# Kernel optimization log

Measured on AMD Instinct MI355X. Metric: run time of the kernel, lower is better.

The kernel has to match this reference:

```python
import jax, jax.numpy as jnp
import numpy as np

B, L, N, M = 2, 4, 2048, 1024
K, DIV = 32, 4
S = K // DIV  # maxpool window along neighbor axis
F1 = 128      # prev features
PF = 64       # lift output point-feature dim
OUT = 256
EPS = 1e-5


def setup_inputs() -> dict:
    key = jax.random.key(0)
    ks = jax.random.split(key, 12)
    C_in = PF + F1  # 192, conv input channels
    return {
        "points": jax.random.normal(ks[0], (B, L, N, 3), jnp.float32),
        "queries": jax.random.normal(ks[1], (B, L, M, 3), jnp.float32),
        "feat_prev": jax.random.normal(ks[2], (B, L, N, F1), jnp.float32),
        # Lift params
        "bn1_g": jnp.ones((3,), jnp.float32),
        "bn1_b": jnp.zeros((3,), jnp.float32),
        "w1": jax.random.normal(ks[3], (PF // 2, 3), jnp.float32) * 0.3,
        "b1": jnp.zeros((PF // 2,), jnp.float32),
        "bn2_g": jnp.ones((PF // 2,), jnp.float32),
        "bn2_b": jnp.zeros((PF // 2,), jnp.float32),
        "w2": jax.random.normal(ks[4], (PF, PF // 2), jnp.float32) * 0.1,
        "b2": jnp.zeros((PF,), jnp.float32),
        # conv = BatchNorm3d(C_in) + Conv3d(C_in, OUT, (1,1,DIV))
        "bnc_g": jnp.ones((C_in,), jnp.float32),
        "bnc_b": jnp.zeros((C_in,), jnp.float32),
        "conv_w": jax.random.normal(ks[5], (OUT, C_in, DIV), jnp.float32) * 0.05,
        "conv_b": jnp.zeros((OUT,), jnp.float32),
    }


def _bn(x, g, b):
    """Training-mode batchnorm, channel = last axis (equivalent to the
    torch transpose(1,4)->BatchNorm3d->transpose(1,4) pattern)."""
    ax = tuple(range(x.ndim - 1))
    m = x.mean(ax)
    v = x.var(ax)  # biased variance, as torch uses for normalization
    return (x - m) * jax.lax.rsqrt(v + EPS) * g + b


_gather = jax.vmap(jax.vmap(lambda arr, idx: arr[idx]))  # over B, L


def reference(points, queries, feat_prev,
              bn1_g, bn1_b, w1, b1, bn2_g, bn2_b, w2, b2,
              bnc_g, bnc_b, conv_w, conv_b):
    # ---- KNN (cdist + topk, fully batched) ----
    pn = jnp.sum(points * points, -1)          # (B,L,N)
    qn = jnp.sum(queries * queries, -1)        # (B,L,M)
    cross = jnp.einsum('blmc,blnc->blmn', queries, points)
    d2 = qn[..., None] + pn[:, :, None, :] - 2.0 * cross  # (B,L,M,N)
    idx = jax.lax.top_k(-d2, K)[1]             # (B,L,M,K) ascending distance

    nn_pts = _gather(points, idx)              # (B,L,M,K,3)
    local = queries[:, :, :, None, :] - nn_pts # center - neighbors

    # ---- Lift MLP (with batchnorm) ----
    h = _bn(local, bn1_g, bn1_b)
    h = jax.nn.relu(jnp.einsum('blmki,oi->blmko', h, w1) + b1)
    h = _bn(h, bn2_g, bn2_b)
    h = jax.nn.relu(jnp.einsum('blmki,oi->blmko', h, w2) + b2)  # (B,L,M,K,PF)

    # ---- gather prev features, concat ----
    fp = _gather(feat_prev, idx)               # (B,L,M,K,F1)
    feat = jnp.concatenate([h, fp], axis=-1)   # (B,L,M,K,C_in)

    # ---- maxpool over neighbor shells: window S, stride S along K ----
    C = feat.shape[-1]
    fm = feat.reshape(B, L, M, DIV, S, C).max(axis=4)  # (B,L,M,DIV,C)

    # ---- BatchNorm3d(C_in) + Conv3d(C_in, OUT, (1,1,DIV)) ----
    fm = _bn(fm, bnc_g, bnc_b)
    out = jnp.einsum('blmdc,ocd->blmo', fm, conv_w) + conv_b  # (B,L,M,OUT)
    return out
```

## Files before the change

kernel.cpp:

```cpp
#include <hip/hip_runtime.h>
#include <cstdint>

#define B_    2
#define L_    4
#define N_    2048
#define M_    1024
#define K_    32
#define DIV_  4
#define S_    8
#define F1_   128
#define PF_   64
#define CIN_  192
#define OUT_  256
#define EPS_  1e-5f

#define BL_   (B_*L_)
#define BLM_  (BL_*M_)
#define NPTS_ (BLM_*K_)
#define ROWS_ (BLM_*DIV_)

#define OFF_FMH  0
#define OFF_IDX  3145728
#define OFF_LOC  3407872
#define OFF_W1F  4456448
#define OFF_B1F  4456544
#define OFF_W2F  4456576
#define OFF_B2F  4458624
#define OFF_WCB  4458688
#define OFF_BCF  4556992
#define OFF_P2   4557248
#define OFF_P3   4573632

typedef __attribute__((ext_vector_type(8))) short short8;
typedef __attribute__((ext_vector_type(4))) short short4v;
typedef __attribute__((ext_vector_type(4))) float f32x4;

__device__ __forceinline__ unsigned short f2bf(float f)
{
    unsigned u = __float_as_uint(f);
    unsigned r = (u + 0x7FFFu + ((u >> 16) & 1u)) >> 16;
    return (unsigned short)r;
}
__device__ __forceinline__ float bf2f(unsigned short h)
{
    unsigned u = ((unsigned)h) << 16;
    return __uint_as_float(u);
}

__device__ __forceinline__ unsigned long long shfl_xor_u64(unsigned long long v, int m)
{
    unsigned lo = (unsigned)v, hi = (unsigned)(v >> 32);
    lo = __shfl_xor(lo, m); hi = __shfl_xor(hi, m);
    return ((unsigned long long)hi << 32) | lo;
}
__device__ __forceinline__ unsigned long long shfl_u64(unsigned long long v, int src)
{
    unsigned lo = (unsigned)v, hi = (unsigned)(v >> 32);
    lo = __shfl(lo, src); hi = __shfl(hi, src);
    return ((unsigned long long)hi << 32) | lo;
}

__global__ __launch_bounds__(512) void k_knn(const float* __restrict__ points,
                                             const float* __restrict__ queries,
                                             int*   __restrict__ idxbuf,
                                             float* __restrict__ local4,
                                             float* __restrict__ p1)
{
#pragma clang fp contract(off)
    __shared__ float4 pt[N_];
    __shared__ unsigned bufA[8][64];
    __shared__ int      bufN[8][64];
    __shared__ float  wred[8][8];

    const int t    = threadIdx.x;
    const int lane = t & 63;
    const int wv   = t >> 6;
    const int bl   = blockIdx.x >> 7;
    const int m    = ((blockIdx.x & 127) << 3) + wv;

    const float* P = points  + (size_t)bl * (N_*3);
    const float* Q = queries + (size_t)bl * (M_*3);

    for (int n = t; n < N_; n += 512) {
        float x = P[n*3], y = P[n*3+1], z = P[n*3+2];
        float pn = (x*x + y*y) + z*z;
        pt[n] = make_float4(x, y, z, pn);
    }
    __syncthreads();

    const float qx = Q[m*3], qy = Q[m*3+1], qz = Q[m*3+2];
    const float qn = (qx*qx + qy*qy) + qz*qz;
    const double qxd = (double)qx, qyd = (double)qy, qzd = (double)qz;

    unsigned           Aa = 0xFFFFFFFFu;
    unsigned long long Ab = ~0ULL;
    unsigned           thrA = 0xFFFFFFFFu;
    int bufcnt = 0;

    auto flushfn = [&]() {
        unsigned sa = 0xFFFFFFFFu; unsigned long long sb = ~0ULL;
        if (lane < bufcnt) {
            sa = bufA[wv][lane];
            const int n = bufN[wv][lane];
            const float4 p4 = pt[n];
            double dx = qxd - (double)p4.x, dy = qyd - (double)p4.y, dz = qzd - (double)p4.z;
            double d2d = dx*dx + dy*dy + dz*dz;
            unsigned long long uB = (unsigned long long)__double_as_longlong(d2d);
            uB = (uB & 0x8000000000000000ULL) ? ~uB : (uB | 0x8000000000000000ULL);
            sb = (uB & ~2047ULL) | (unsigned long long)n;
        }
        for (int k = 2; k <= 64; k <<= 1) {
            for (int j = k >> 1; j >= 1; j >>= 1) {
                unsigned           pa = __shfl_xor(sa, j);
                unsigned long long pb = shfl_xor_u64(sb, j);
                bool pl = (pa < sa) || (pa == sa && pb < sb);
                bool wantMin = (((lane & k) == 0) == ((lane & j) == 0));
                if (pl == wantMin) { sa = pa; sb = pb; }
            }
        }
        int src = (31 - lane) & 63;
        unsigned           ba  = __shfl(sa, src);
        unsigned long long bb2 = shfl_u64(sb, src);
        if (lane < 32) {
            bool bless = (ba < Aa) || (ba == Aa && bb2 < Ab);
            if (bless) { Aa = ba; Ab = bb2; }
        }
        for (int j = 16; j >= 1; j >>= 1) {
            unsigned           pa = __shfl_xor(Aa, j);
            unsigned long long pb = shfl_xor_u64(Ab, j);
            bool pl = (pa < Aa) || (pa == Aa && pb < Ab);
            bool wantMin = ((lane & j) == 0);
            if (pl == wantMin) { Aa = pa; Ab = pb; }
        }
        bufcnt = 0;
        thrA = __shfl(Aa, 31);
    };

    for (int r = 0; r < 32; ++r) {
        const int n = r*64 + lane;
        const float4 p4 = pt[n];
        float cross = (qx*p4.x + qy*p4.y) + qz*p4.z;
        float d2f = (qn + p4.w) - 2.0f*cross;
        unsigned uA = __float_as_uint(d2f);
        uA = (uA & 0x80000000u) ? ~uA : (uA | 0x80000000u);

        bool lt = (uA <= thrA);
        unsigned long long mask = __ballot(lt);
        int cnt = __builtin_popcountll(mask);
        if (cnt == 0) continue;
        if (bufcnt + cnt > 64) {
            flushfn();
            lt = (uA <= thrA);
            mask = __ballot(lt);
            cnt = __builtin_popcountll(mask);
            if (cnt == 0) continue;
        }
        int pos = bufcnt + __builtin_popcountll(mask & ((1ULL << lane) - 1ULL));
        if (lt) { bufA[wv][pos] = uA; bufN[wv][pos] = n; }
        bufcnt += cnt;
    }
    if (bufcnt > 0) flushfn();

    const long long base = ((long long)bl * M_ + m) * K_;
    float lx = 0.f, ly = 0.f, lz = 0.f;
    if (lane < 32) {
        const int n = (int)(Ab & 2047ULL);
        idxbuf[base + lane] = n;
        const float4 p4 = pt[n];
        lx = qx - p4.x; ly = qy - p4.y; lz = qz - p4.z;
        *(float4*)(local4 + (base + lane)*4) = make_float4(lx, ly, lz, 0.f);
    }
    float s0 = lx, s1 = ly, s2 = lz, s3 = lx*lx, s4 = ly*ly, s5 = lz*lz;
#pragma unroll
    for (int off = 32; off; off >>= 1) {
        s0 += __shfl_xor(s0, off); s1 += __shfl_xor(s1, off); s2 += __shfl_xor(s2, off);
        s3 += __shfl_xor(s3, off); s4 += __shfl_xor(s4, off); s5 += __shfl_xor(s5, off);
    }
    if (lane == 0) {
        wred[wv][0]=s0; wred[wv][1]=s1; wred[wv][2]=s2;
        wred[wv][3]=s3; wred[wv][4]=s4; wred[wv][5]=s5;
    }
    __syncthreads();
    if (t < 6) {
        float s = 0.f;
#pragma unroll
        for (int w = 0; w < 8; ++w) s += wred[w][t];
        p1[(long long)blockIdx.x*8 + t] = s;
    }
}

__global__ __launch_bounds__(256) void k_fold1(const float* __restrict__ p1,
                        const float* __restrict__ w1, const float* __restrict__ b1,
                        const float* __restrict__ g,  const float* __restrict__ bb,
                        float* __restrict__ w1f, float* __restrict__ b1f)
{
    __shared__ float red[6][33];
    __shared__ float s1[3], t1[3];
    const int t = threadIdx.x;
    const int c = t >> 5, i = t & 31;
    if (c < 6) {
        float s = 0.f;
        for (int w = i; w < 1024; w += 32) s += p1[w*8 + c];
        red[c][i] = s;
    }
    __syncthreads();
    if (t < 3) {
        float S = 0.f, Q = 0.f;
        for (int k = 0; k < 32; ++k) { S += red[t][k]; Q += red[t+3][k]; }
        float mean = S / (float)NPTS_;
        float var  = Q / (float)NPTS_ - mean*mean;
        float r = 1.0f / sqrtf(var + EPS_);
        float sc = r * g[t];
        s1[t] = sc; t1[t] = bb[t] - mean*sc;
    }
    __syncthreads();
    if (t < 32) {
        float acc = b1[t];
        for (int i2 = 0; i2 < 3; ++i2) {
            float w = w1[t*3+i2];
            w1f[t*3+i2] = w * s1[i2];
            acc += w * t1[i2];
        }
        b1f[t] = acc;
    }
}

__global__ __launch_bounds__(256) void k_stats2(const float* __restrict__ local4,
                                                const float* __restrict__ w1f,
                                                const float* __restrict__ b1f,
                                                float* __restrict__ p2)
{
    __shared__ float4 pts[1024];
    __shared__ float  sred[4][64];
    const int t = threadIdx.x;
    const int lane = t & 63;
    const int wv   = t >> 6;
    const int base = blockIdx.x * 1024;

    for (int j = t; j < 1024; j += 256)
        pts[j] = *(const float4*)(local4 + (size_t)(base + j) * 4);

    const int ch = lane & 31;
    const float w0 = w1f[ch*3], w1v = w1f[ch*3+1], w2v = w1f[ch*3+2];
    const float bv = b1f[ch];
    __syncthreads();

    float s = 0.f, q = 0.f;
    const int pbase = wv*256 + (lane >> 5);
    for (int it = 0; it < 128; ++it) {
        float4 v = pts[pbase + it*2];
        float h = fmaxf(bv + w0*v.x + w1v*v.y + w2v*v.z, 0.f);
        s += h; q += h*h;
    }
    s += __shfl_xor(s, 32); q += __shfl_xor(q, 32);
    if (lane < 32) { sred[wv][lane] = s; sred[wv][32+lane] = q; }
    __syncthreads();
    if (t < 64)
        p2[blockIdx.x*64 + t] = sred[0][t]+sred[1][t]+sred[2][t]+sred[3][t];
}

__global__ void k_fold2(const float* __restrict__ p2,
                        const float* __restrict__ w2, const float* __restrict__ b2,
                        const float* __restrict__ g,  const float* __restrict__ bb,
                        float* __restrict__ w2f, float* __restrict__ b2f)
{
    __shared__ float s2[32], t2[32];
    int t = threadIdx.x;
    if (t < 32) {
        float S = 0, Q = 0;
        for (int b = 0; b < 256; ++b) { S += p2[b*64+t]; Q += p2[b*64+32+t]; }
        float mean = S / (float)NPTS_;
        float var  = Q / (float)NPTS_ - mean*mean;
        float r = 1.0f / sqrtf(var + EPS_);
        float sc = r * g[t];
        s2[t] = sc; t2[t] = bb[t] - mean*sc;
    }
    __syncthreads();
    float acc = b2[t];
    for (int i = 0; i < 32; ++i) {
        float w = w2[t*32+i];
        w2f[t*32+i] = w * s2[i];
        acc += w * t2[i];
    }
    b2f[t] = acc;
}

__global__ __launch_bounds__(256) void k_shell(const float* __restrict__ feat_prev,
                                               const int*   __restrict__ idxbuf,
                                               const float* __restrict__ local4,
                                               const float* __restrict__ w1f,
                                               const float* __restrict__ b1f,
                                               const float* __restrict__ w2f,
                                               const float* __restrict__ b2f,
                                               unsigned short* __restrict__ fmh)
{
    __shared__ float w1s[96], b1s[32];
    __shared__ float w2s[64][33];
    __shared__ int   idxs[K_];
    __shared__ float locs[K_][4];
    __shared__ __align__(16) float h1s[K_][36];
    __shared__ float fmrow[DIV_][CIN_];

    const int t = threadIdx.x;
    const int lane = t & 63;
    const int wv   = t >> 6;
    const int blm = blockIdx.x;
    const long long base = (long long)blm * K_;

    for (int j = t; j < 96; j += 256) w1s[j] = w1f[j];
    if (t < 32) b1s[t] = b1f[t];
    for (int j = t; j < 2048; j += 256) { int o = j >> 5, i = j & 31; w2s[o][i] = w2f[j]; }
    if (t < 32)  idxs[t] = idxbuf[base + t];
    if (t < 128) ((float*)locs)[t] = local4[base*4 + t];
    __syncthreads();

    for (int j = t; j < 1024; j += 256) {
        int k = j >> 5, o = j & 31;
        float v = b1s[o] + w1s[o*3]*locs[k][0] + w1s[o*3+1]*locs[k][1] + w1s[o*3+2]*locs[k][2];
        h1s[k][o] = fmaxf(v, 0.f);
    }
    __syncthreads();

    {
        float w2c[32];
#pragma unroll
        for (int i = 0; i < 32; ++i) w2c[i] = w2s[lane][i];
        const float b2v = b2f[lane];
        float mx = 0.0f;
#pragma unroll
        for (int kk = 0; kk < 8; ++kk) {
            const int k = wv*8 + kk;
            const float4* hp = (const float4*)&h1s[k][0];
            float acc = b2v;
#pragma unroll
            for (int c = 0; c < 8; ++c) {
                float4 h4 = hp[c];
                acc += h4.x*w2c[c*4+0];
                acc += h4.y*w2c[c*4+1];
                acc += h4.z*w2c[c*4+2];
                acc += h4.w*w2c[c*4+3];
            }
            mx = fmaxf(mx, fmaxf(acc, 0.f));
        }
        fmrow[wv][lane] = mx;
    }
    {
        const float* fp0 = feat_prev + (size_t)(blm / M_) * N_ * F1_;
#pragma unroll
        for (int ph = 0; ph < 2; ++ph) {
            int d = ph*2 + (t >> 7), c = t & 127;
            float mx = -3.4e38f;
#pragma unroll
            for (int j = 0; j < 8; ++j) {
                int n = idxs[d*8+j];
                mx = fmaxf(mx, fp0[(size_t)n*F1_ + c]);
            }
            fmrow[d][64 + c] = mx;
        }
    }
    __syncthreads();
    for (int j = t; j < DIV_*CIN_; j += 256)
        fmh[(size_t)blm * (DIV_*CIN_) + j] = f2bf((&fmrow[0][0])[j]);
}

__global__ void k_stats3(const unsigned short* __restrict__ fmh, float* __restrict__ p3)
{
    const int t = threadIdx.x;
    const int blk = blockIdx.x;
    float s = 0.f, q = 0.f;
    const size_t base = (size_t)blk * 256 * CIN_;
    for (int r = 0; r < 256; ++r) {
        float v = bf2f(fmh[base + (size_t)r*CIN_ + t]);
        s += v; q += v*v;
    }
    p3[blk*384 + t] = s;
    p3[blk*384 + 192 + t] = q;
}

__global__ __launch_bounds__(256) void k_fold3(const float* __restrict__ p3,
                                               const float* __restrict__ conv_w,
                                               const float* __restrict__ conv_b,
                                               const float* __restrict__ g,
                                               const float* __restrict__ bb,
                                               unsigned short* __restrict__ wcfb,
                                               float* __restrict__ bcf)
{
    __shared__ float sc[CIN_], tc[CIN_];
    const int t = threadIdx.x;
    if (t < CIN_) {
        float S = 0, Q = 0;
        for (int b = 0; b < 128; ++b) { S += p3[b*384+t]; Q += p3[b*384+192+t]; }
        float mean = S / (float)ROWS_;
        float var  = Q / (float)ROWS_ - mean*mean;
        float r = 1.0f / sqrtf(var + EPS_);
        float s = r * g[t];
        sc[t] = s; tc[t] = bb[t] - mean*s;
    }
    __syncthreads();
    const int lo = blockIdx.x * 3072;
    for (int j = lo + t; j < lo + 3072; j += 256) {
        int o = j / 768, k = j - o*768;
        int d = k / CIN_, c = k - d*CIN_;
        wcfb[j] = f2bf(conv_w[o*768 + c*4 + d] * sc[c]);
    }
    if (blockIdx.x == 0) {
        float acc = conv_b[t];
        for (int c = 0; c < CIN_; ++c) {
            float tcv = tc[c];
#pragma unroll
            for (int d = 0; d < 4; ++d) acc += tcv * conv_w[t*768 + c*4 + d];
        }
        bcf[t] = acc;
    }
}

__global__ __launch_bounds__(256) void k_gemm(const unsigned short* __restrict__ A,
                                              const unsigned short* __restrict__ Wb,
                                              const float* __restrict__ bias,
                                              float* __restrict__ C)
{
    __shared__ __align__(16) unsigned short As[128][72];
    __shared__ __align__(16) unsigned short Bs[64][72];
    const int t = threadIdx.x;
    const int lane = t & 63;
    const int wv = t >> 6;
    const int row0 = (blockIdx.x >> 2) * 128;
    const int col0 = (blockIdx.x & 3) * 64;
    const int wr = wv >> 1, wc = wv & 1;
    const int r16 = lane & 15, kq = lane >> 4;

    f32x4 acc[4][2];
#pragma unroll
    for (int i = 0; i < 4; ++i)
#pragma unroll
        for (int j = 0; j < 2; ++j) acc[i][j] = (f32x4){0.f,0.f,0.f,0.f};

    for (int kt = 0; kt < 12; ++kt) {
#pragma unroll
        for (int p = 0; p < 4; ++p) {
            int j = p*256 + t;
            int r = j >> 3, kc = (j & 7) * 8;
            *(short8*)&As[r][kc] = *(const short8*)(A + (size_t)(row0 + r)*768 + kt*64 + kc);
        }
#pragma unroll
        for (int p = 0; p < 2; ++p) {
            int j = p*256 + t;
            int r = j >> 3, kc = (j & 7) * 8;
            *(short8*)&Bs[r][kc] = *(const short8*)(Wb + (size_t)(col0 + r)*768 + kt*64 + kc);
        }
        __syncthreads();
#pragma unroll
        for (int ks = 0; ks < 2; ++ks) {
            short8 bf[2];
#pragma unroll
            for (int n = 0; n < 2; ++n) {
                const unsigned short* pb = &Bs[wc*32 + n*16 + r16][ks*32 + kq*4];
                short4v b0 = *(const short4v*)pb;
                short4v b1 = *(const short4v*)(pb + 16);
                bf[n][0]=b0[0]; bf[n][1]=b0[1]; bf[n][2]=b0[2]; bf[n][3]=b0[3];
                bf[n][4]=b1[0]; bf[n][5]=b1[1]; bf[n][6]=b1[2]; bf[n][7]=b1[3];
            }
#pragma unroll
            for (int mf = 0; mf < 4; ++mf) {
                const unsigned short* pa = &As[wr*64 + mf*16 + r16][ks*32 + kq*4];
                short4v a0 = *(const short4v*)pa;
                short4v a1 = *(const short4v*)(pa + 16);
                short8 af;
                af[0]=a0[0]; af[1]=a0[1]; af[2]=a0[2]; af[3]=a0[3];
                af[4]=a1[0]; af[5]=a1[1]; af[6]=a1[2]; af[7]=a1[3];
                acc[mf][0] = __builtin_amdgcn_mfma_f32_16x16x32_bf16(af, bf[0], acc[mf][0], 0, 0, 0);
                acc[mf][1] = __builtin_amdgcn_mfma_f32_16x16x32_bf16(af, bf[1], acc[mf][1], 0, 0, 0);
            }
        }
        __syncthreads();
    }

#pragma unroll
    for (int mf = 0; mf < 4; ++mf) {
#pragma unroll
        for (int n = 0; n < 2; ++n) {
            const int col = col0 + wc*32 + n*16 + r16;
            const float bv = bias[col];
#pragma unroll
            for (int i = 0; i < 4; ++i) {
                int row = row0 + wr*64 + mf*16 + kq*4 + i;
                C[(size_t)row*256 + col] = acc[mf][n][i] + bv;
            }
        }
    }
}

extern "C" void kernel_launch(void* const* d_in, const int* in_sizes, int n_in,
                              void* d_out, int out_size, void* d_ws, size_t ws_size,
                              hipStream_t stream)
{
    const float* points    = (const float*)d_in[0];
    const float* queries   = (const float*)d_in[1];
    const float* feat_prev = (const float*)d_in[2];
    const float* bn1g = (const float*)d_in[3];
    const float* bn1b = (const float*)d_in[4];
    const float* w1   = (const float*)d_in[5];
    const float* b1   = (const float*)d_in[6];
    const float* bn2g = (const float*)d_in[7];
    const float* bn2b = (const float*)d_in[8];
    const float* w2   = (const float*)d_in[9];
    const float* b2   = (const float*)d_in[10];
    const float* bncg = (const float*)d_in[11];
    const float* bncb = (const float*)d_in[12];
    const float* convw= (const float*)d_in[13];
    const float* convb= (const float*)d_in[14];

    float* ws   = (float*)d_ws;
    unsigned short* fmh = (unsigned short*)(ws + OFF_FMH);
    int*   idxb = (int*)(ws + OFF_IDX);
    float* loc4 = ws + OFF_LOC;
    float* w1f  = ws + OFF_W1F;
    float* b1f  = ws + OFF_B1F;
    float* w2f  = ws + OFF_W2F;
    float* b2f  = ws + OFF_B2F;
    unsigned short* wcfb = (unsigned short*)(ws + OFF_WCB);
    float* bcf  = ws + OFF_BCF;
    float* p1   = ws + OFF_FMH;
    float* p2   = ws + OFF_P2;
    float* p3   = ws + OFF_P3;

    k_knn   <<<1024, 512, 0, stream>>>(points, queries, idxb, loc4, p1);
    k_fold1 <<<1, 256, 0, stream>>>(p1, w1, b1, bn1g, bn1b, w1f, b1f);
    k_stats2<<<256, 256, 0, stream>>>(loc4, w1f, b1f, p2);
    k_fold2 <<<1, 64, 0, stream>>>(p2, w2, b2, bn2g, bn2b, w2f, b2f);
    k_shell <<<BLM_, 256, 0, stream>>>(feat_prev, idxb, loc4, w1f, b1f, w2f, b2f, fmh);
    k_stats3<<<128, 192, 0, stream>>>(fmh, p3);
    k_fold3 <<<64, 256, 0, stream>>>(p3, convw, convb, bncg, bncb, wcfb, bcf);
    k_gemm  <<<256, 256, 0, stream>>>(fmh, wcfb, bcf, (float*)d_out);
}
```

Measured before the change: 178.5 us.

## Slim KNN sort keys, prefetch points, drop shell smem staging, widen stats3 grid

The KNN bitonic merge now carries a 32-bit float key plus index instead of a 64-bit double key. The double-precision key is recomputed only when a wave-wide ballot finds real ties. The point loop software-prefetches the next float4 from shared memory. k_shell drops its shared-memory staging of w2 and the fmrow buffer: it reads w2 rows as float4 directly from global and writes bf16 results straight out, which removes a barrier and the copy loop. k_stats3 runs on twice as many blocks with half the rows each, and k_fold3 sums the larger partial array; this adds ballot branches in the sort and uncoalesced per-lane w2 loads.

```diff
diff --git a/kernel.cpp b/kernel.cpp
--- a/kernel.cpp
+++ b/kernel.cpp
@@ -47,19 +47,6 @@
     return __uint_as_float(u);
 }
 
-__device__ __forceinline__ unsigned long long shfl_xor_u64(unsigned long long v, int m)
-{
-    unsigned lo = (unsigned)v, hi = (unsigned)(v >> 32);
-    lo = __shfl_xor(lo, m); hi = __shfl_xor(hi, m);
-    return ((unsigned long long)hi << 32) | lo;
-}
-__device__ __forceinline__ unsigned long long shfl_u64(unsigned long long v, int src)
-{
-    unsigned lo = (unsigned)v, hi = (unsigned)(v >> 32);
-    lo = __shfl(lo, src); hi = __shfl(hi, src);
-    return ((unsigned long long)hi << 32) | lo;
-}
-
 __global__ __launch_bounds__(512) void k_knn(const float* __restrict__ points,
                                              const float* __restrict__ queries,
                                              int*   __restrict__ idxbuf,
@@ -69,7 +56,7 @@
 #pragma clang fp contract(off)
     __shared__ float4 pt[N_];
     __shared__ unsigned bufA[8][64];
-    __shared__ int      bufN[8][64];
+    __shared__ unsigned bufN[8][64];
     __shared__ float  wred[8][8];
 
     const int t    = threadIdx.x;
@@ -92,57 +79,71 @@
     const float qn = (qx*qx + qy*qy) + qz*qz;
     const double qxd = (double)qx, qyd = (double)qy, qzd = (double)qz;
 
-    unsigned           Aa = 0xFFFFFFFFu;
-    unsigned long long Ab = ~0ULL;
-    unsigned           thrA = 0xFFFFFFFFu;
+    auto uBkey = [&](unsigned n) -> unsigned long long {
+        const float4 p4 = pt[n & 2047];
+        double dx = qxd - (double)p4.x, dy = qyd - (double)p4.y, dz = qzd - (double)p4.z;
+        double d2d = dx*dx + dy*dy + dz*dz;
+        unsigned long long uB = (unsigned long long)__double_as_longlong(d2d);
+        uB = (uB & 0x8000000000000000ULL) ? ~uB : (uB | 0x8000000000000000ULL);
+        return (uB & ~2047ULL) | (unsigned long long)(n & 2047);
+    };
+    auto cmp_less = [&](unsigned pa, unsigned pn, unsigned ca, unsigned cn) -> bool {
+        bool eq = (pa == ca);
+        bool pl = eq ? (pn < cn) : (pa < ca);
+        bool realtie = eq && (ca != 0xFFFFFFFFu);
+        if (__ballot(realtie)) {
+            unsigned long long pb = uBkey(pn);
+            unsigned long long cb = uBkey(cn);
+            if (realtie) pl = (pb < cb);
+        }
+        return pl;
+    };
+
+    unsigned Aa = 0xFFFFFFFFu;
+    unsigned An = 2048u + lane;
+    unsigned thrA = 0xFFFFFFFFu;
     int bufcnt = 0;
 
     auto flushfn = [&]() {
-        unsigned sa = 0xFFFFFFFFu; unsigned long long sb = ~0ULL;
-        if (lane < bufcnt) {
-            sa = bufA[wv][lane];
-            const int n = bufN[wv][lane];
-            const float4 p4 = pt[n];
-            double dx = qxd - (double)p4.x, dy = qyd - (double)p4.y, dz = qzd - (double)p4.z;
-            double d2d = dx*dx + dy*dy + dz*dz;
-            unsigned long long uB = (unsigned long long)__double_as_longlong(d2d);
-            uB = (uB & 0x8000000000000000ULL) ? ~uB : (uB | 0x8000000000000000ULL);
-            sb = (uB & ~2047ULL) | (unsigned long long)n;
-        }
+        unsigned sa, sn;
+        if (lane < bufcnt) { sa = bufA[wv][lane]; sn = bufN[wv][lane]; }
+        else               { sa = 0xFFFFFFFFu;    sn = 2048u + lane; }
         for (int k = 2; k <= 64; k <<= 1) {
             for (int j = k >> 1; j >= 1; j >>= 1) {
-                unsigned           pa = __shfl_xor(sa, j);
-                unsigned long long pb = shfl_xor_u64(sb, j);
-                bool pl = (pa < sa) || (pa == sa && pb < sb);
+                unsigned pa = __shfl_xor(sa, j);
+                unsigned pn = __shfl_xor(sn, j);
                 bool wantMin = (((lane & k) == 0) == ((lane & j) == 0));
-                if (pl == wantMin) { sa = pa; sb = pb; }
+                bool pl = cmp_less(pa, pn, sa, sn);
+                if (pl == wantMin) { sa = pa; sn = pn; }
             }
         }
         int src = (31 - lane) & 63;
-        unsigned           ba  = __shfl(sa, src);
-        unsigned long long bb2 = shfl_u64(sb, src);
+        unsigned ba = __shfl(sa, src);
+        unsigned bn = __shfl(sn, src);
         if (lane < 32) {
-            bool bless = (ba < Aa) || (ba == Aa && bb2 < Ab);
-            if (bless) { Aa = ba; Ab = bb2; }
+            if (cmp_less(ba, bn, Aa, An)) { Aa = ba; An = bn; }
         }
         for (int j = 16; j >= 1; j >>= 1) {
-            unsigned           pa = __shfl_xor(Aa, j);
-            unsigned long long pb = shfl_xor_u64(Ab, j);
-            bool pl = (pa < Aa) || (pa == Aa && pb < Ab);
+            unsigned pa = __shfl_xor(Aa, j);
+            unsigned pn = __shfl_xor(An, j);
             bool wantMin = ((lane & j) == 0);
-            if (pl == wantMin) { Aa = pa; Ab = pb; }
+            bool pl = cmp_less(pa, pn, Aa, An);
+            if (pl == wantMin) { Aa = pa; An = pn; }
         }
         bufcnt = 0;
         thrA = __shfl(Aa, 31);
     };
 
+    float4 p4 = pt[lane];
     for (int r = 0; r < 32; ++r) {
         const int n = r*64 + lane;
-        const float4 p4 = pt[n];
+        float4 p4n = p4;
+        if (r < 31) p4n = pt[n + 64];
         float cross = (qx*p4.x + qy*p4.y) + qz*p4.z;
         float d2f = (qn + p4.w) - 2.0f*cross;
         unsigned uA = __float_as_uint(d2f);
         uA = (uA & 0x80000000u) ? ~uA : (uA | 0x80000000u);
+        p4 = p4n;
 
         bool lt = (uA <= thrA);
         unsigned long long mask = __ballot(lt);
@@ -156,7 +157,7 @@
             if (cnt == 0) continue;
         }
         int pos = bufcnt + __builtin_popcountll(mask & ((1ULL << lane) - 1ULL));
-        if (lt) { bufA[wv][pos] = uA; bufN[wv][pos] = n; }
+        if (lt) { bufA[wv][pos] = uA; bufN[wv][pos] = (unsigned)n; }
         bufcnt += cnt;
     }
     if (bufcnt > 0) flushfn();
@@ -164,10 +165,10 @@
     const long long base = ((long long)bl * M_ + m) * K_;
     float lx = 0.f, ly = 0.f, lz = 0.f;
     if (lane < 32) {
-        const int n = (int)(Ab & 2047ULL);
+        const int n = (int)An;
         idxbuf[base + lane] = n;
-        const float4 p4 = pt[n];
-        lx = qx - p4.x; ly = qy - p4.y; lz = qz - p4.z;
+        const float4 pp = pt[n];
+        lx = qx - pp.x; ly = qy - pp.y; lz = qz - pp.z;
         *(float4*)(local4 + (base + lane)*4) = make_float4(lx, ly, lz, 0.f);
     }
     float s0 = lx, s1 = ly, s2 = lz, s3 = lx*lx, s4 = ly*ly, s5 = lz*lz;
@@ -295,11 +296,9 @@
                                                unsigned short* __restrict__ fmh)
 {
     __shared__ float w1s[96], b1s[32];
-    __shared__ float w2s[64][33];
     __shared__ int   idxs[K_];
     __shared__ float locs[K_][4];
     __shared__ __align__(16) float h1s[K_][36];
-    __shared__ float fmrow[DIV_][CIN_];
 
     const int t = threadIdx.x;
     const int lane = t & 63;
@@ -307,10 +306,9 @@
     const int blm = blockIdx.x;
     const long long base = (long long)blm * K_;
 
-    for (int j = t; j < 96; j += 256) w1s[j] = w1f[j];
-    if (t < 32) b1s[t] = b1f[t];
-    for (int j = t; j < 2048; j += 256) { int o = j >> 5, i = j & 31; w2s[o][i] = w2f[j]; }
-    if (t < 32)  idxs[t] = idxbuf[base + t];
+    if (t < 96)  w1s[t] = w1f[t];
+    if (t >= 96 && t < 128) b1s[t-96] = b1f[t-96];
+    if (t >= 128 && t < 160) idxs[t-128] = idxbuf[base + (t-128)];
     if (t < 128) ((float*)locs)[t] = local4[base*4 + t];
     __syncthreads();
 
@@ -324,7 +322,10 @@
     {
         float w2c[32];
 #pragma unroll
-        for (int i = 0; i < 32; ++i) w2c[i] = w2s[lane][i];
+        for (int i = 0; i < 8; ++i) {
+            float4 v = *(const float4*)(w2f + lane*32 + i*4);
+            w2c[i*4]=v.x; w2c[i*4+1]=v.y; w2c[i*4+2]=v.z; w2c[i*4+3]=v.w;
+        }
         const float b2v = b2f[lane];
         float mx = 0.0f;
 #pragma unroll
@@ -342,7 +343,7 @@
             }
             mx = fmaxf(mx, fmaxf(acc, 0.f));
         }
-        fmrow[wv][lane] = mx;
+        fmh[(size_t)blm*(DIV_*CIN_) + wv*CIN_ + lane] = f2bf(mx);
     }
     {
         const float* fp0 = feat_prev + (size_t)(blm / M_) * N_ * F1_;
@@ -355,12 +356,9 @@
                 int n = idxs[d*8+j];
                 mx = fmaxf(mx, fp0[(size_t)n*F1_ + c]);
             }
-            fmrow[d][64 + c] = mx;
-        }
-    }
-    __syncthreads();
-    for (int j = t; j < DIV_*CIN_; j += 256)
-        fmh[(size_t)blm * (DIV_*CIN_) + j] = f2bf((&fmrow[0][0])[j]);
+            fmh[(size_t)blm*(DIV_*CIN_) + d*CIN_ + 64 + c] = f2bf(mx);
+        }
+    }
 }
 
 __global__ void k_stats3(const unsigned short* __restrict__ fmh, float* __restrict__ p3)
@@ -368,8 +366,8 @@
     const int t = threadIdx.x;
     const int blk = blockIdx.x;
     float s = 0.f, q = 0.f;
-    const size_t base = (size_t)blk * 256 * CIN_;
-    for (int r = 0; r < 256; ++r) {
+    const size_t base = (size_t)blk * 128 * CIN_;
+    for (int r = 0; r < 128; ++r) {
         float v = bf2f(fmh[base + (size_t)r*CIN_ + t]);
         s += v; q += v*v;
     }
@@ -389,7 +387,7 @@
     const int t = threadIdx.x;
     if (t < CIN_) {
         float S = 0, Q = 0;
-        for (int b = 0; b < 128; ++b) { S += p3[b*384+t]; Q += p3[b*384+192+t]; }
+        for (int b = 0; b < 256; ++b) { S += p3[b*384+t]; Q += p3[b*384+192+t]; }
         float mean = S / (float)ROWS_;
         float var  = Q / (float)ROWS_ - mean*mean;
         float r = 1.0f / sqrtf(var + EPS_);
@@ -529,7 +527,7 @@
     k_stats2<<<256, 256, 0, stream>>>(loc4, w1f, b1f, p2);
     k_fold2 <<<1, 64, 0, stream>>>(p2, w2, b2, bn2g, bn2b, w2f, b2f);
     k_shell <<<BLM_, 256, 0, stream>>>(feat_prev, idxb, loc4, w1f, b1f, w2f, b2f, fmh);
-    k_stats3<<<128, 192, 0, stream>>>(fmh, p3);
+    k_stats3<<<256, 192, 0, stream>>>(fmh, p3);
     k_fold3 <<<64, 256, 0, stream>>>(p3, convw, convb, bncg, bncb, wcfb, bcf);
     k_gemm  <<<256, 256, 0, stream>>>(fmh, wcfb, bcf, (float*)d_out);
 }
```

Result: slower. 183.8 us (+2.9%).
